# Kernel optimization log

Hardware: AMD Instinct MI355X
Metric: run time of the kernel (lower is better)

## Reference

```python
import jax, jax.numpy as jnp
import numpy as np

B, T, D = 512, 200, 64
VU, VI = 100000, 200000


def _init_params():
    ks = jax.random.split(jax.random.key(1), 12)
    g = lambda k, s, sc=0.05: jax.random.normal(k, s, dtype=jnp.float32) * sc
    return {
        "emb_user": g(ks[0], (VU, D)),
        "emb_item": g(ks[1], (VI, D)),
        "gru_Wx": g(ks[2], (D, 3 * D)),
        "gru_Wh": g(ks[3], (D, 3 * D)),
        "gru_b": jnp.zeros((3 * D,), jnp.float32),
        "aug_Wx": g(ks[4], (D, 3 * D)),
        "aug_Wh": g(ks[5], (D, 3 * D)),
        "aug_b": jnp.zeros((3 * D,), jnp.float32),
        "aux_W1": g(ks[6], (2 * D, 100)),
        "aux_b1": jnp.zeros((100,), jnp.float32),
        "aux_W2": g(ks[7], (100, 50)),
        "aux_b2": jnp.zeros((50,), jnp.float32),
        "aux_W3": g(ks[8], (50, 2)),
        "aux_b3": jnp.zeros((2,), jnp.float32),
        "bn_gamma": jnp.ones((2 * D,), jnp.float32),
        "bn_beta": jnp.zeros((2 * D,), jnp.float32),
        "fc_W1": g(ks[9], (2 * D, 200)),
        "fc_b1": jnp.zeros((200,), jnp.float32),
        "prelu_a1": jnp.zeros((200,), jnp.float32),
        "fc_W2": g(ks[10], (200, 80)),
        "fc_b2": jnp.zeros((80,), jnp.float32),
        "prelu_a2": jnp.zeros((80,), jnp.float32),
        "fc_W3": g(ks[11], (80, 2)),
        "fc_b3": jnp.zeros((2,), jnp.float32),
    }


def setup_inputs():
    key = jax.random.key(0)
    k1, k2, k3 = jax.random.split(key, 3)
    inp = {
        "user_ids": jax.random.randint(k1, (B,), 0, VU),
        "behavior_ids": jax.random.randint(k2, (B, T), 0, VI),
        "target_ids": jax.random.randint(k3, (B,), 0, VI),
    }
    inp.update(_init_params())
    return inp


def _gru(x, Wx, Wh, b):
    # x: [B,T,D]; precompute all input-side gate projections, scan over time
    xg = jnp.einsum("btd,de->bte", x, Wx) + b  # [B,T,3D]

    def step(h, xg_t):
        hg = h @ Wh[:, : 2 * D]
        z = jax.nn.sigmoid(xg_t[:, :D] + hg[:, :D])
        r = jax.nn.sigmoid(xg_t[:, D : 2 * D] + hg[:, D:])
        n = jnp.tanh(xg_t[:, 2 * D :] + (r * h) @ Wh[:, 2 * D :])
        h_new = z * h + (1.0 - z) * n
        return h_new, h_new

    h0 = jnp.zeros((x.shape[0], D), x.dtype)
    _, hs = jax.lax.scan(step, h0, jnp.swapaxes(xg, 0, 1))
    return jnp.swapaxes(hs, 0, 1)  # [B,T,D]


def _augru(x, att, Wx, Wh, b):
    # AUGRU: update gate scaled by attention score; returns final hidden [B,D]
    xg = jnp.einsum("btd,de->bte", x, Wx) + b

    def step(h, inputs):
        xg_t, a_t = inputs
        hg = h @ Wh[:, : 2 * D]
        u = jax.nn.sigmoid(xg_t[:, :D] + hg[:, :D])
        r = jax.nn.sigmoid(xg_t[:, D : 2 * D] + hg[:, D:])
        n = jnp.tanh(xg_t[:, 2 * D :] + (r * h) @ Wh[:, 2 * D :])
        u = a_t[:, None] * u
        h_new = (1.0 - u) * h + u * n
        return h_new, None

    h0 = jnp.zeros((x.shape[0], D), x.dtype)
    h, _ = jax.lax.scan(step, h0, (jnp.swapaxes(xg, 0, 1), att.T))
    return h


def _prelu(x, a):
    return jnp.maximum(x, 0.0) + a * jnp.minimum(x, 0.0)


def _forward(user_ids, behavior_ids, target_ids, p):
    user_emb = p["emb_user"][user_ids]          # [B,D]
    beh_emb = p["emb_item"][behavior_ids]       # [B,T,D]
    tgt_emb = p["emb_item"][target_ids]         # [B,D]

    gru_out = _gru(beh_emb, p["gru_Wx"], p["gru_Wh"], p["gru_b"])  # [B,T,D]

    # auxiliary loss: small MLP on (hidden, behavior emb) pairs, click class prob
    aux_in = jnp.concatenate([gru_out, beh_emb], axis=-1)  # [B,T,2D]
    h1 = jax.nn.relu(aux_in @ p["aux_W1"] + p["aux_b1"])
    h2 = jax.nn.relu(h1 @ p["aux_W2"] + p["aux_b2"])
    aux_logits = h2 @ p["aux_W3"] + p["aux_b3"]  # [B,T,2]
    aux_loss = -jnp.mean(jax.nn.log_softmax(aux_logits, axis=-1)[..., 0])

    # target-item attention over GRU hidden states (softmax over time)
    scores = jnp.einsum("bd,btd->bt", tgt_emb, gru_out)
    att = jax.nn.softmax(scores, axis=-1)  # [B,T]

    h_final = _augru(gru_out, att, p["aug_Wx"], p["aug_Wh"], p["aug_b"])  # [B,D]

    join = jnp.concatenate([h_final, user_emb], axis=-1)  # [B,2D]
    mu = jnp.mean(join, axis=0)
    var = jnp.var(join, axis=0)
    x = (join - mu) * jax.lax.rsqrt(var + 1e-3) * p["bn_gamma"] + p["bn_beta"]
    x = _prelu(jax.nn.relu(x @ p["fc_W1"] + p["fc_b1"]), p["prelu_a1"])
    x = _prelu(jax.nn.relu(x @ p["fc_W2"] + p["fc_b2"]), p["prelu_a2"])
    logit = x @ p["fc_W3"] + p["fc_b3"]  # [B,2]
    output = jax.nn.softmax(logit, axis=-1)
    return output, logit, aux_loss


def reference(user_ids, behavior_ids, target_ids, emb_user, emb_item, gru_Wx, gru_Wh, gru_b, aug_Wx, aug_Wh, aug_b, aux_W1, aux_b1, aux_W2, aux_b2, aux_W3, aux_b3, bn_gamma, bn_beta, fc_W1, fc_b1, prelu_a1, fc_W2, fc_b2, prelu_a2, fc_W3, fc_b3):
    p = dict(emb_user=emb_user, emb_item=emb_item, gru_Wx=gru_Wx, gru_Wh=gru_Wh, gru_b=gru_b,
             aug_Wx=aug_Wx, aug_Wh=aug_Wh, aug_b=aug_b, aux_W1=aux_W1, aux_b1=aux_b1,
             aux_W2=aux_W2, aux_b2=aux_b2, aux_W3=aux_W3, aux_b3=aux_b3,
             bn_gamma=bn_gamma, bn_beta=bn_beta, fc_W1=fc_W1, fc_b1=fc_b1, prelu_a1=prelu_a1,
             fc_W2=fc_W2, fc_b2=fc_b2, prelu_a2=prelu_a2, fc_W3=fc_W3, fc_b3=fc_b3)
    return _forward(user_ids, behavior_ids, target_ids, p)
```

## Files before the change

kernel.cpp:

```cpp
#include <hip/hip_runtime.h>
#include <hip/hip_bf16.h>
#include <math.h>

#define BB 512
#define TT 200
#define DD 64
#define G3 192
#define BT (BB*TT)

typedef __hip_bfloat16 bf16;
typedef short short8 __attribute__((ext_vector_type(8)));
typedef float f32x4 __attribute__((ext_vector_type(4)));

__device__ __forceinline__ float b2f(bf16 v){ return __bfloat162float(v); }
__device__ __forceinline__ float sigm(float x){ x = fminf(fmaxf(x,-30.f),30.f); return 1.f/(1.f+__expf(-x)); }
__device__ __forceinline__ float tanh_(float x){ x = fminf(fmaxf(x,-15.f),15.f); float e=__expf(2.f*x); return (e-1.f)/(e+1.f); }

__device__ __forceinline__ float ldv(const void* p, long i, int isbf){
  if (isbf) return __bfloat162float(((const bf16*)p)[i]);
  return ((const float*)p)[i];
}
__device__ __forceinline__ short f2bs(float f){
  union { bf16 b; short s; } u; u.b = __float2bfloat16(f); return u.s;
}
__device__ __forceinline__ float bs2f(short s){
  union { unsigned u; float f; } x; x.u = ((unsigned)(unsigned short)s) << 16; return x.f;
}
__device__ __forceinline__ float rdlane(float v, int l){
  return __int_as_float(__builtin_amdgcn_readlane(__float_as_int(v), l));
}

__global__ void k_probe(const void* gamma, int* flag){
  if (threadIdx.x==0 && blockIdx.x==0)
    flag[0] = (((const unsigned*)gamma)[0] == 0x3F803F80u) ? 1 : 0;
}

__global__ __launch_bounds__(256) void k_prep(const void* W1, const void* W2, const void* b1,
    const void* b2, const void* W3, const void* b3, const void* gruWx, const void* augWx,
    short* w1t, short* w2t, float* b1f, float* b2f, float* w3f, float* b3f,
    short* wxg, short* wxa, const int* flagp){
  int isbf = *flagp;
  int gid = blockIdx.x*256 + threadIdx.x;
  int gstride = gridDim.x*256;
  for (int i = gid; i < 112*128; i += gstride){
    int n = i >> 7, k = i & 127;
    w1t[i] = f2bs((n < 100) ? ldv(W1, (long)k*100 + n, isbf) : 0.f);
  }
  for (int i = gid; i < 64*128; i += gstride){
    int n = i >> 7, k = i & 127;
    w2t[i] = f2bs((n < 50 && k < 100) ? ldv(W2, (long)k*50 + n, isbf) : 0.f);
  }
  for (int i = gid; i < 12288; i += gstride){
    int j = i & 7, L = (i >> 3) & 63, tk = i >> 9;
    int tile = tk >> 1, kb = tk & 1;
    int k = kb*32 + (L>>4)*8 + j, col = tile*16 + (L & 15);
    wxg[i] = f2bs(ldv(gruWx, (long)k*G3 + col, isbf));
    wxa[i] = f2bs(ldv(augWx, (long)k*G3 + col, isbf));
  }
  if (gid < 112) b1f[gid] = (gid < 100) ? ldv(b1, gid, isbf) : 0.f;
  if (gid < 64)  b2f[gid] = (gid < 50)  ? ldv(b2, gid, isbf) : 0.f;
  if (gid < 100) w3f[gid] = ldv(W3, gid, isbf);
  if (gid < 2)   b3f[gid] = ldv(b3, gid, isbf);
}

__global__ void k_gather(const int* __restrict__ uid, const int* __restrict__ tgt_id,
                         const void* __restrict__ eu, const void* __restrict__ ei,
                         float* __restrict__ tgt, float* __restrict__ usr, const int* flagp){
  int b = blockIdx.x, j = threadIdx.x;
  int isbf = *flagp;
  tgt[b*DD+j] = ldv(ei, (long)tgt_id[b]*DD + j, isbf);
  usr[b*DD+j] = ldv(eu, (long)uid[b]*DD + j, isbf);
}

template<bool GATHER>
__global__ __launch_bounds__(256) void k_xg(const short* __restrict__ wxf, const void* __restrict__ bias,
        const void* __restrict__ emb, const int* __restrict__ ids, const float* __restrict__ Ain,
        float* __restrict__ out, const int* flagp){
  __shared__ __align__(16) char lds[58112];
  int isbf = *flagp;
  int tid = threadIdx.x;
  long rbase = (long)blockIdx.x * 128;
  for (int i = tid; i < 1536; i += 256)
    *(short8*)(lds + i*16) = *(const short8*)(wxf + i*8);
  float* sB = (float*)(lds + 57344);
  if (tid < G3) sB[tid] = ldv(bias, tid, isbf);
  for (int u = tid; u < 1024; u += 256){
    int row = u >> 3, slot = u & 7;
    int off = row*128 + slot*16; off ^= (row&7)<<4;
    if (GATHER){
      long e = (long)ids[rbase+row]*DD + slot*8;
      short8 v;
      if (isbf) v = *(const short8*)((const short*)emb + e);
      else {
        const float* g = (const float*)emb + e;
        f32x4 f0 = *(const f32x4*)g;
        f32x4 f1 = *(const f32x4*)(g+4);
        v[0]=f2bs(f0[0]); v[1]=f2bs(f0[1]); v[2]=f2bs(f0[2]); v[3]=f2bs(f0[3]);
        v[4]=f2bs(f1[0]); v[5]=f2bs(f1[1]); v[6]=f2bs(f1[2]); v[7]=f2bs(f1[3]);
      }
      *(short8*)(lds + 24576 + off) = v;
    } else {
      const float* g = Ain + (rbase+row)*DD + slot*8;
      f32x4 f0 = *(const f32x4*)g;
      f32x4 f1 = *(const f32x4*)(g+4);
      short8 hi, lo;
      #pragma unroll
      for (int q=0;q<4;q++){
        hi[q] = f2bs(f0[q]); lo[q] = f2bs(f0[q] - bs2f(hi[q]));
        hi[4+q] = f2bs(f1[q]); lo[4+q] = f2bs(f1[q] - bs2f(hi[4+q]));
      }
      *(short8*)(lds + 24576 + off) = hi;
      *(short8*)(lds + 40960 + off) = lo;
    }
  }
  __syncthreads();
  int lane = tid & 63, w = tid >> 6;
  int m0 = w*32, lr = lane & 15, lg = lane >> 4;
  f32x4 acc[2][12];
  #pragma unroll
  for (int mi=0;mi<2;mi++){
    #pragma unroll
    for (int nt=0;nt<12;nt++){ acc[mi][nt][0]=0.f; acc[mi][nt][1]=0.f; acc[mi][nt][2]=0.f; acc[mi][nt][3]=0.f; }
  }
  #pragma unroll
  for (int ks=0; ks<2; ks++){
    short8 ah[2], al[2];
    #pragma unroll
    for (int mi=0; mi<2; mi++){
      int row = m0 + mi*16 + lr;
      int off = row*128 + ks*64 + lg*16; off ^= (row&7)<<4;
      ah[mi] = *(const short8*)(lds + 24576 + off);
      if (!GATHER) al[mi] = *(const short8*)(lds + 40960 + off);
    }
    #pragma unroll
    for (int nt=0; nt<12; nt++){
      short8 bf = *(const short8*)(lds + ((nt*2+ks)*64 + lane)*16);
      #pragma unroll
      for (int mi=0; mi<2; mi++){
        if (!GATHER) acc[mi][nt] = __builtin_amdgcn_mfma_f32_16x16x32_bf16(al[mi], bf, acc[mi][nt], 0,0,0);
        acc[mi][nt] = __builtin_amdgcn_mfma_f32_16x16x32_bf16(ah[mi], bf, acc[mi][nt], 0,0,0);
      }
    }
  }
  int r4 = lg*4;
  #pragma unroll
  for (int mi=0;mi<2;mi++){
    #pragma unroll
    for (int nt=0;nt<12;nt++){
      int n = nt*16 + lr;
      float bv = sB[n];
      #pragma unroll
      for (int i=0;i<4;i++){
        long row = rbase + m0 + mi*16 + r4 + i;
        out[row*G3 + n] = acc[mi][nt][i] + bv;
      }
    }
  }
}

template<bool AUG>
__global__ __launch_bounds__(64,1) void k_scan(const float* __restrict__ xg, const void* __restrict__ Whv,
    const float* __restrict__ att, float* __restrict__ hs_out, float* __restrict__ h_final,
    const int* flagp){
  int b = blockIdx.x, j = threadIdx.x;
  int isbf = *flagp;
  float whz[64], whr[64], whn[64];
  if (isbf){
    const bf16* Wh = (const bf16*)Whv;
    #pragma unroll
    for (int d=0; d<64; d++){
      whz[d] = b2f(Wh[d*G3 + j]);
      whr[d] = b2f(Wh[d*G3 + 64 + j]);
      whn[d] = b2f(Wh[d*G3 + 128 + j]);
    }
  } else {
    const float* Wh = (const float*)Whv;
    #pragma unroll
    for (int d=0; d<64; d++){
      whz[d] = Wh[d*G3 + j];
      whr[d] = Wh[d*G3 + 64 + j];
      whn[d] = Wh[d*G3 + 128 + j];
    }
  }
  float hj = 0.f;
  const float* xgb = xg + (size_t)b*TT*G3 + j;
  const float* attb = att + (size_t)b*TT;
  float xz = xgb[0], xr = xgb[64], xn = xgb[128];
  float at = AUG ? attb[0] : 0.f;
  for (int t=0; t<TT; t++){
    int tp = (t+1 < TT) ? t+1 : t;
    const float* q = xgb + (size_t)tp*G3;
    float nxz = q[0], nxr = q[64], nxn = q[128];
    float nat = AUG ? attb[tp] : 0.f;
    float az0=0.f,az1=0.f,az2=0.f,az3=0.f, ar0=0.f,ar1=0.f,ar2=0.f,ar3=0.f;
    #pragma unroll
    for (int d=0; d<64; d+=4){
      float h0=rdlane(hj,d+0), h1=rdlane(hj,d+1), h2=rdlane(hj,d+2), h3=rdlane(hj,d+3);
      az0+=h0*whz[d+0]; az1+=h1*whz[d+1]; az2+=h2*whz[d+2]; az3+=h3*whz[d+3];
      ar0+=h0*whr[d+0]; ar1+=h1*whr[d+1]; ar2+=h2*whr[d+2]; ar3+=h3*whr[d+3];
    }
    float z = sigm(xz + ((az0+az1)+(az2+az3)));
    float r = sigm(xr + ((ar0+ar1)+(ar2+ar3)));
    float u = AUG ? (at*z) : z;
    float rh = r*hj;
    float an0=0.f,an1=0.f,an2=0.f,an3=0.f;
    #pragma unroll
    for (int d=0; d<64; d+=4){
      float r0=rdlane(rh,d+0), r1=rdlane(rh,d+1), r2=rdlane(rh,d+2), r3=rdlane(rh,d+3);
      an0+=r0*whn[d+0]; an1+=r1*whn[d+1]; an2+=r2*whn[d+2]; an3+=r3*whn[d+3];
    }
    float n = tanh_(xn + ((an0+an1)+(an2+an3)));
    float hnew = AUG ? ((1.f-u)*hj + u*n) : (u*hj + (1.f-u)*n);
    hj = hnew;
    if (!AUG) hs_out[((size_t)b*TT + t)*DD + j] = hnew;
    xz=nxz; xr=nxr; xn=nxn; at=nat;
  }
  if (AUG) h_final[b*DD + j] = hj;
}

__global__ __launch_bounds__(256) void k_att(const float* __restrict__ gru, const float* __restrict__ tgt,
                                             float* __restrict__ att){
  int b = blockIdx.x, tid = threadIdx.x;
  __shared__ float st[DD];
  __shared__ float red[256];
  if (tid < DD) st[tid] = tgt[b*DD + tid];
  __syncthreads();
  float s = 0.f;
  if (tid < TT){
    const float* g = gru + ((size_t)b*TT + tid)*DD;
    #pragma unroll
    for (int d=0; d<DD; d++) s += g[d]*st[d];
  }
  red[tid] = (tid<TT) ? s : -1e30f;
  __syncthreads();
  for (int w=128; w>0; w>>=1){ if (tid<w) red[tid] = fmaxf(red[tid], red[tid+w]); __syncthreads(); }
  float m = red[0];
  __syncthreads();
  float e = (tid<TT) ? __expf(s - m) : 0.f;
  red[tid] = e; __syncthreads();
  for (int w=128; w>0; w>>=1){ if (tid<w) red[tid] += red[tid+w]; __syncthreads(); }
  float inv = 1.f/red[0];
  if (tid < TT) att[b*TT + tid] = e*inv;
}

__global__ __launch_bounds__(256) void k_aux(const float* __restrict__ gru, const void* __restrict__ emb,
    const int* __restrict__ ids, const short* __restrict__ w1t, const short* __restrict__ w2t,
    const float* __restrict__ b1f, const float* __restrict__ b2f, const float* __restrict__ w3f,
    const float* __restrict__ b3f, float* __restrict__ part, const int* flagp){
  __shared__ __align__(16) char smem[78976];
  float* sb1 = (float*)(smem + 77824);
  float* sb2 = (float*)(smem + 78272);
  float* sw3 = (float*)(smem + 78528);
  float* sb3 = (float*)(smem + 78928);
  float* wred= (float*)(smem + 78936);
  int tid = threadIdx.x;
  int isbf = *flagp;
  long rbase = (long)blockIdx.x * 128;

  for (int i = tid; i < 1792; i += 256){
    int n = i >> 4, slot = i & 15;
    short8 v = *(const short8*)(w1t + n*128 + slot*8);
    int off = n*256 + slot*16; off ^= (n&7)<<4;
    *(short8*)(smem + 32768 + off) = v;
  }
  for (int i = tid; i < 1024; i += 256){
    int n = i >> 4, slot = i & 15;
    short8 v = *(const short8*)(w2t + n*128 + slot*8);
    int off = n*256 + slot*16; off ^= (n&7)<<4;
    *(short8*)(smem + 61440 + off) = v;
  }
  if (tid < 112) sb1[tid] = b1f[tid];
  if (tid < 100) sw3[tid] = w3f[tid];
  if (tid >= 112 && tid < 176) sb2[tid-112] = b2f[tid-112];
  if (tid >= 176 && tid < 178) sb3[tid-176] = b3f[tid-176];
  for (int i = tid; i < 2048; i += 256){
    int row = i >> 4, slot = i & 15, k0 = slot*8;
    short8 v;
    if (k0 < 64){
      const float* g = gru + (rbase+row)*64 + k0;
      f32x4 f0 = *(const f32x4*)g;
      f32x4 f1 = *(const f32x4*)(g+4);
      v[0]=f2bs(f0[0]); v[1]=f2bs(f0[1]); v[2]=f2bs(f0[2]); v[3]=f2bs(f0[3]);
      v[4]=f2bs(f1[0]); v[5]=f2bs(f1[1]); v[6]=f2bs(f1[2]); v[7]=f2bs(f1[3]);
    } else {
      long e = (long)ids[rbase+row]*64 + (k0-64);
      if (isbf){
        v = *(const short8*)((const short*)emb + e);
      } else {
        const float* g = (const float*)emb + e;
        f32x4 f0 = *(const f32x4*)g;
        f32x4 f1 = *(const f32x4*)(g+4);
        v[0]=f2bs(f0[0]); v[1]=f2bs(f0[1]); v[2]=f2bs(f0[2]); v[3]=f2bs(f0[3]);
        v[4]=f2bs(f1[0]); v[5]=f2bs(f1[1]); v[6]=f2bs(f1[2]); v[7]=f2bs(f1[3]);
      }
    }
    int off = row*256 + slot*16; off ^= (row&7)<<4;
    *(short8*)(smem + off) = v;
  }
  __syncthreads();

  int lane = tid & 63;
  int wv = tid >> 6;
  int m0 = wv * 32;
  int lrow = lane & 15;
  int kbL = ((lane >> 4) * 8) * 2;

  f32x4 acc1[2][7];
  #pragma unroll
  for (int mi=0;mi<2;mi++){
    #pragma unroll
    for (int ni=0;ni<7;ni++){ acc1[mi][ni][0]=0.f; acc1[mi][ni][1]=0.f; acc1[mi][ni][2]=0.f; acc1[mi][ni][3]=0.f; }
  }
  #pragma unroll
  for (int ks=0; ks<4; ks++){
    int kb = ks*64 + kbL;
    short8 af[2], bfv[7];
    #pragma unroll
    for (int mi=0; mi<2; mi++){
      int row = m0 + mi*16 + lrow;
      int off = row*256 + kb; off ^= (row&7)<<4;
      af[mi] = *(const short8*)(smem + off);
    }
    #pragma unroll
    for (int ni=0; ni<7; ni++){
      int n = ni*16 + lrow;
      int off = n*256 + kb; off ^= (n&7)<<4;
      bfv[ni] = *(const short8*)(smem + 32768 + off);
    }
    #pragma unroll
    for (int mi=0; mi<2; mi++){
      #pragma unroll
      for (int ni=0; ni<7; ni++)
        acc1[mi][ni] = __builtin_amdgcn_mfma_f32_16x16x32_bf16(af[mi], bfv[ni], acc1[mi][ni], 0, 0, 0);
    }
  }
  int lr4 = (lane >> 4) * 4;
  #pragma unroll
  for (int mi=0; mi<2; mi++){
    #pragma unroll
    for (int ni=0; ni<7; ni++){
      int col = ni*16 + lrow;
      float bias = sb1[col];
      #pragma unroll
      for (int i=0;i<4;i++){
        int row = m0 + mi*16 + lr4 + i;
        float v = fmaxf(acc1[mi][ni][i] + bias, 0.f);
        int off = row*256 + col*2; off ^= (row&7)<<4;
        *(short*)(smem + off) = f2bs(v);
      }
    }
  }
  {
    int row = m0 + (lane >> 1);
    int off = row*256 + (112 + (lane&1)*8)*2; off ^= (row&7)<<4;
    short8 z = {0,0,0,0,0,0,0,0};
    *(short8*)(smem + off) = z;
  }
  __syncthreads();

  f32x4 acc2[2][4];
  #pragma unroll
  for (int mi=0;mi<2;mi++){
    #pragma unroll
    for (int ni=0;ni<4;ni++){ acc2[mi][ni][0]=0.f; acc2[mi][ni][1]=0.f; acc2[mi][ni][2]=0.f; acc2[mi][ni][3]=0.f; }
  }
  #pragma unroll
  for (int ks=0; ks<4; ks++){
    int kb = ks*64 + kbL;
    short8 af[2], bgv[4];
    #pragma unroll
    for (int mi=0; mi<2; mi++){
      int row = m0 + mi*16 + lrow;
      int off = row*256 + kb; off ^= (row&7)<<4;
      af[mi] = *(const short8*)(smem + off);
    }
    #pragma unroll
    for (int ni=0; ni<4; ni++){
      int n = ni*16 + lrow;
      int off = n*256 + kb; off ^= (n&7)<<4;
      bgv[ni] = *(const short8*)(smem + 61440 + off);
    }
    #pragma unroll
    for (int mi=0; mi<2; mi++){
      #pragma unroll
      for (int ni=0; ni<4; ni++)
        acc2[mi][ni] = __builtin_amdgcn_mfma_f32_16x16x32_bf16(af[mi], bgv[ni], acc2[mi][ni], 0, 0, 0);
    }
  }
  #pragma unroll
  for (int mi=0; mi<2; mi++){
    #pragma unroll
    for (int ni=0; ni<4; ni++){
      int col = ni*16 + lrow;
      float bias = sb2[col];
      #pragma unroll
      for (int i=0;i<4;i++){
        int row = m0 + mi*16 + lr4 + i;
        float v = fmaxf(acc2[mi][ni][i] + bias, 0.f);
        *(short*)(smem + 32768 + row*136 + col*2) = f2bs(v);
      }
    }
  }
  __syncthreads();

  int row = tid >> 1, half = tid & 1;
  const short* h2r = (const short*)(smem + 32768) + row*68;
  float p0 = 0.f, p1 = 0.f;
  int kb0 = half*32, kb1 = half ? 50 : 32;
  for (int k=kb0; k<kb1; k++){
    float h = bs2f(h2r[k]);
    p0 += h*sw3[2*k]; p1 += h*sw3[2*k+1];
  }
  p0 += __shfl_xor(p0, 1, 64);
  p1 += __shfl_xor(p1, 1, 64);
  float l0 = p0 + sb3[0], l1 = p1 + sb3[1];
  float mx = fmaxf(l0, l1);
  float lse = mx + logf(__expf(l0-mx) + __expf(l1-mx));
  float c = (lse - l0) * 0.5f;
  #pragma unroll
  for (int off=32; off; off>>=1) c += __shfl_down(c, off, 64);
  if (lane == 0) wred[wv] = c;
  __syncthreads();
  if (tid == 0) part[blockIdx.x] = wred[0]+wred[1]+wred[2]+wred[3];
}

__global__ void k_auxred(const float* __restrict__ part, float* __restrict__ total){
  __shared__ float red[256];
  int tid = threadIdx.x;
  float s = 0.f;
  for (int i=tid; i<800; i+=256) s += part[i];
  red[tid]=s; __syncthreads();
  for (int w=128;w;w>>=1){ if(tid<w) red[tid]+=red[tid+w]; __syncthreads(); }
  if (tid==0) total[0]=red[0];
}

__global__ __launch_bounds__(64) void k_bn(const float* __restrict__ hf, const float* __restrict__ usr,
                                           float* __restrict__ bn){
  int c = blockIdx.x, l = threadIdx.x;
  const float* src = (c<64) ? (hf + c) : (usr + (c-64));
  float s=0.f, q=0.f;
  for (int r=l; r<BB; r+=64){ float v = src[(size_t)r*DD]; s+=v; q+=v*v; }
  #pragma unroll
  for (int off=32; off; off>>=1){ s += __shfl_down(s,off,64); q += __shfl_down(q,off,64); }
  if (l==0){
    float mean = s*(1.f/BB);
    float var = fmaxf(q*(1.f/BB) - mean*mean, 0.f);
    bn[c] = mean;
    bn[128+c] = rsqrtf(var + 1e-3f);
  }
}

template<typename WT>
__device__ __forceinline__ void fc_body(int b, int tid, const float* hf, const float* usr, const float* bn,
   const WT* gamma, const WT* beta, const WT* W1, const WT* b1, const WT* W2, const WT* b2,
   const WT* W3, const WT* b3, const float* auxsum, void* outv, int obf,
   float* xn, float* y1, float* y2){
  for (int c=tid; c<128; c+=64){
    float v = (c<64) ? hf[b*DD+c] : usr[b*DD + c-64];
    xn[c] = (v - bn[c])*bn[128+c]*b2f(gamma[c]) + b2f(beta[c]);
  }
  __syncthreads();
  #pragma unroll
  for (int i=0;i<4;i++){
    int n = tid + i*64;
    if (n < 200){
      float a = b2f(b1[n]);
      for (int k=0;k<128;k++) a += xn[k]*b2f(W1[k*200+n]);
      y1[n] = fmaxf(a, 0.f);
    }
  }
  __syncthreads();
  #pragma unroll
  for (int i=0;i<2;i++){
    int n = tid + i*64;
    if (n < 80){
      float a = b2f(b2[n]);
      for (int k=0;k<200;k++) a += y1[k]*b2f(W2[k*80+n]);
      y2[n] = fmaxf(a, 0.f);
    }
  }
  __syncthreads();
  float hv = y2[tid];
  float p0 = hv*b2f(W3[tid*2+0]);
  float p1 = hv*b2f(W3[tid*2+1]);
  if (tid < 16){
    float h2 = y2[tid+64];
    p0 += h2*b2f(W3[(tid+64)*2+0]);
    p1 += h2*b2f(W3[(tid+64)*2+1]);
  }
  #pragma unroll
  for (int off=32; off; off>>=1){ p0 += __shfl_down(p0,off,64); p1 += __shfl_down(p1,off,64); }
  if (tid==0){
    float l0 = p0 + b2f(b3[0]), l1 = p1 + b2f(b3[1]);
    float m = fmaxf(l0,l1);
    float e0 = __expf(l0-m), e1 = __expf(l1-m);
    float inv = 1.f/(e0+e1);
    float q0 = e0*inv, q1 = e1*inv;
    float al = auxsum[0] * (1.f/(float)BT);
    if (obf){
      bf16* o = (bf16*)outv;
      o[b*2+0] = __float2bfloat16(q0); o[b*2+1] = __float2bfloat16(q1);
      o[1024 + b*2+0] = __float2bfloat16(l0); o[1024 + b*2+1] = __float2bfloat16(l1);
      if (b==0) o[2048] = __float2bfloat16(al);
    } else {
      float* o = (float*)outv;
      o[b*2+0] = q0; o[b*2+1] = q1;
      o[1024 + b*2+0] = l0; o[1024 + b*2+1] = l1;
      if (b==0) o[2048] = al;
    }
  }
}

__global__ __launch_bounds__(64) void k_fc(const float* __restrict__ hf, const float* __restrict__ usr,
   const float* __restrict__ bn, const void* gamma, const void* beta,
   const void* W1, const void* b1, const void* W2, const void* b2,
   const void* W3, const void* b3, const float* __restrict__ auxsum,
   void* outv, const int* flagp){
  __shared__ float xn[128], y1[200], y2[80];
  int b = blockIdx.x, tid = threadIdx.x;
  int isbf = *flagp;
  if (isbf)
    fc_body<bf16>(b,tid,hf,usr,bn,(const bf16*)gamma,(const bf16*)beta,(const bf16*)W1,(const bf16*)b1,
                  (const bf16*)W2,(const bf16*)b2,(const bf16*)W3,(const bf16*)b3,auxsum,outv,1,xn,y1,y2);
  else
    fc_body<float>(b,tid,hf,usr,bn,(const float*)gamma,(const float*)beta,(const float*)W1,(const float*)b1,
                  (const float*)W2,(const float*)b2,(const float*)W3,(const float*)b3,auxsum,outv,0,xn,y1,y2);
}

extern "C" void kernel_launch(void* const* d_in, const int* in_sizes, int n_in,
                              void* d_out, int out_size, void* d_ws, size_t ws_size,
                              hipStream_t stream) {
  const int*  user_ids     = (const int*) d_in[0];
  const int*  behavior_ids = (const int*) d_in[1];
  const int*  target_ids   = (const int*) d_in[2];
  const void* emb_user = d_in[3];
  const void* emb_item = d_in[4];
  const void* gru_Wx   = d_in[5];
  const void* gru_Wh   = d_in[6];
  const void* gru_b    = d_in[7];
  const void* aug_Wx   = d_in[8];
  const void* aug_Wh   = d_in[9];
  const void* aug_b    = d_in[10];
  const void* aux_W1   = d_in[11];
  const void* aux_b1   = d_in[12];
  const void* aux_W2   = d_in[13];
  const void* aux_b2   = d_in[14];
  const void* aux_W3   = d_in[15];
  const void* aux_b3   = d_in[16];
  const void* bn_gamma = d_in[17];
  const void* bn_beta  = d_in[18];
  const void* fc_W1    = d_in[19];
  const void* fc_b1    = d_in[20];
  const void* fc_W2    = d_in[22];
  const void* fc_b2    = d_in[23];
  const void* fc_W3    = d_in[25];
  const void* fc_b3    = d_in[26];

  float* ws = (float*)d_ws;
  const size_t FLAG_OFF = 0;
  const size_t XG_OFF   = 16;
  const size_t GRU_OFF  = XG_OFF  + (size_t)BT*G3;
  const size_t ATT_OFF  = GRU_OFF + (size_t)BT*DD;
  const size_t TGT_OFF  = ATT_OFF + (size_t)BT;
  const size_t USR_OFF  = TGT_OFF + (size_t)BB*DD;
  const size_t HF_OFF   = USR_OFF + (size_t)BB*DD;
  const size_t BN_OFF   = HF_OFF  + (size_t)BB*DD;
  const size_t AUXP_OFF = BN_OFF  + 256;
  const size_t AUXS_OFF = AUXP_OFF + 800;
  const size_t W1T_OFF  = AUXS_OFF + 16;
  const size_t W2T_OFF  = W1T_OFF + 7168;
  const size_t B1F_OFF  = W2T_OFF + 4096;
  const size_t B2F_OFF  = B1F_OFF + 112;
  const size_t W3F_OFF  = B2F_OFF + 64;
  const size_t B3F_OFF  = W3F_OFF + 100;
  const size_t WXG_OFF  = B3F_OFF + 4;
  const size_t WXA_OFF  = WXG_OFF + 6144;
  const size_t END_OFF  = WXA_OFF + 6144;
  if (ws_size < END_OFF*sizeof(float)) return;

  int*   flag = (int*)(ws + FLAG_OFF);
  float* xg   = ws + XG_OFF;
  float* gruo = ws + GRU_OFF;
  float* att  = ws + ATT_OFF;
  float* tgt  = ws + TGT_OFF;
  float* usr  = ws + USR_OFF;
  float* hf   = ws + HF_OFF;
  float* bnst = ws + BN_OFF;
  float* auxp = ws + AUXP_OFF;
  float* auxs = ws + AUXS_OFF;
  short* w1t  = (short*)(ws + W1T_OFF);
  short* w2t  = (short*)(ws + W2T_OFF);
  float* b1f  = ws + B1F_OFF;
  float* b2f  = ws + B2F_OFF;
  float* w3f  = ws + W3F_OFF;
  float* b3f  = ws + B3F_OFF;
  short* wxg  = (short*)(ws + WXG_OFF);
  short* wxa  = (short*)(ws + WXA_OFF);

  k_probe<<<1, 64, 0, stream>>>(bn_gamma, flag);
  k_prep<<<8, 256, 0, stream>>>(aux_W1, aux_W2, aux_b1, aux_b2, aux_W3, aux_b3, gru_Wx, aug_Wx,
                                w1t, w2t, b1f, b2f, w3f, b3f, wxg, wxa, flag);
  k_gather<<<BB, 64, 0, stream>>>(user_ids, target_ids, emb_user, emb_item, tgt, usr, flag);
  k_xg<true><<<BT/128, 256, 0, stream>>>(wxg, gru_b, emb_item, behavior_ids, nullptr, xg, flag);
  k_scan<false><<<BB, 64, 0, stream>>>(xg, gru_Wh, nullptr, gruo, nullptr, flag);
  k_att<<<BB, 256, 0, stream>>>(gruo, tgt, att);
  k_aux<<<BT/128, 256, 0, stream>>>(gruo, emb_item, behavior_ids, w1t, w2t, b1f, b2f, w3f, b3f, auxp, flag);
  k_auxred<<<1, 256, 0, stream>>>(auxp, auxs);
  k_xg<false><<<BT/128, 256, 0, stream>>>(wxa, aug_b, nullptr, nullptr, gruo, xg, flag);
  k_scan<true><<<BB, 64, 0, stream>>>(xg, aug_Wh, att, nullptr, hf, flag);
  k_bn<<<128, 64, 0, stream>>>(hf, usr, bnst);
  k_fc<<<BB, 64, 0, stream>>>(hf, usr, bnst, bn_gamma, bn_beta, fc_W1, fc_b1, fc_W2, fc_b2, fc_W3, fc_b3, auxs, d_out, flag);
}
```

Before: 451.2 us.

## Compute GRU/AUGRU recurrent matvec with bf16 MFMA instead of readlane FMAs

The per-timestep recurrent h@Wh product in the scan kernel moves from scalar readlane broadcasts plus FMAs to MFMA 16x16x32 bf16 instructions. Wh is held in registers as bf16 fragments, and the hidden state is rearranged into A-fragments with ds_bpermute and rounded to bf16. Only one row of each 16x16 output is used, so most of the MFMA work is wasted. Rounding h and Wh to bf16 inside the recurrence also lowers precision and may let error build up over 200 steps.

```diff
diff --git a/kernel.cpp b/kernel.cpp
--- a/kernel.cpp
+++ b/kernel.cpp
@@ -26,8 +26,26 @@
 __device__ __forceinline__ float bs2f(short s){
   union { unsigned u; float f; } x; x.u = ((unsigned)(unsigned short)s) << 16; return x.f;
 }
-__device__ __forceinline__ float rdlane(float v, int l){
-  return __int_as_float(__builtin_amdgcn_readlane(__float_as_int(v), l));
+__device__ __forceinline__ unsigned pk2(int a, int b){
+  return (((unsigned)a + 0x8000u) >> 16) | (((unsigned)b + 0x8000u) & 0xffff0000u);
+}
+__device__ __forceinline__ short8 gfrag(int bits, int base){
+  int v0 = __builtin_amdgcn_ds_bpermute(base+ 0, bits);
+  int v1 = __builtin_amdgcn_ds_bpermute(base+ 4, bits);
+  int v2 = __builtin_amdgcn_ds_bpermute(base+ 8, bits);
+  int v3 = __builtin_amdgcn_ds_bpermute(base+12, bits);
+  int v4 = __builtin_amdgcn_ds_bpermute(base+16, bits);
+  int v5 = __builtin_amdgcn_ds_bpermute(base+20, bits);
+  int v6 = __builtin_amdgcn_ds_bpermute(base+24, bits);
+  int v7 = __builtin_amdgcn_ds_bpermute(base+28, bits);
+  union { unsigned u[4]; short8 s; } cv;
+  cv.u[0] = pk2(v0,v1); cv.u[1] = pk2(v2,v3); cv.u[2] = pk2(v4,v5); cv.u[3] = pk2(v6,v7);
+  return cv.s;
+}
+__device__ __forceinline__ float sel4(float a0, float a1, float a2, float a3, int lg){
+  float x01 = (lg & 1) ? a1 : a0;
+  float x23 = (lg & 1) ? a3 : a2;
+  return (lg & 2) ? x23 : x01;
 }
 
 __global__ void k_probe(const void* gamma, int* flag){
@@ -162,60 +180,86 @@
 __global__ __launch_bounds__(64,1) void k_scan(const float* __restrict__ xg, const void* __restrict__ Whv,
     const float* __restrict__ att, float* __restrict__ hs_out, float* __restrict__ h_final,
     const int* flagp){
-  int b = blockIdx.x, j = threadIdx.x;
+  int lane = threadIdx.x;
+  int b = blockIdx.x;
   int isbf = *flagp;
-  float whz[64], whr[64], whn[64];
-  if (isbf){
-    const bf16* Wh = (const bf16*)Whv;
-    #pragma unroll
-    for (int d=0; d<64; d++){
-      whz[d] = b2f(Wh[d*G3 + j]);
-      whr[d] = b2f(Wh[d*G3 + 64 + j]);
-      whn[d] = b2f(Wh[d*G3 + 128 + j]);
-    }
-  } else {
-    const float* Wh = (const float*)Whv;
-    #pragma unroll
-    for (int d=0; d<64; d++){
-      whz[d] = Wh[d*G3 + j];
-      whr[d] = Wh[d*G3 + 64 + j];
-      whn[d] = Wh[d*G3 + 128 + j];
+  int lr = lane & 15, lg = lane >> 4;
+  short8 wzf[4][2], wrf[4][2], wnf[4][2];
+  #pragma unroll
+  for (int ti=0; ti<4; ti++){
+    #pragma unroll
+    for (int kb=0; kb<2; kb++){
+      short8 z8, r8, n8;
+      #pragma unroll
+      for (int jj=0; jj<8; jj++){
+        long k = kb*32 + lg*8 + jj;
+        int cz = ti*16 + lr, cr = 64 + ti*16 + lr, cn = 128 + ti*16 + lr;
+        if (isbf){
+          const short* Wh = (const short*)Whv;
+          z8[jj] = Wh[k*G3 + cz]; r8[jj] = Wh[k*G3 + cr]; n8[jj] = Wh[k*G3 + cn];
+        } else {
+          const float* Wh = (const float*)Whv;
+          z8[jj] = f2bs(Wh[k*G3 + cz]); r8[jj] = f2bs(Wh[k*G3 + cr]); n8[jj] = f2bs(Wh[k*G3 + cn]);
+        }
+      }
+      wzf[ti][kb] = z8; wrf[ti][kb] = r8; wnf[ti][kb] = n8;
     }
   }
   float hj = 0.f;
-  const float* xgb = xg + (size_t)b*TT*G3 + j;
+  const float* xgb = xg + (size_t)b*TT*G3;
   const float* attb = att + (size_t)b*TT;
-  float xz = xgb[0], xr = xgb[64], xn = xgb[128];
+  float xz = xgb[lane], xr = xgb[64+lane], xn = xgb[128+lane];
   float at = AUG ? attb[0] : 0.f;
+  int abase = lg*32;
   for (int t=0; t<TT; t++){
     int tp = (t+1 < TT) ? t+1 : t;
-    const float* q = xgb + (size_t)tp*G3;
-    float nxz = q[0], nxr = q[64], nxn = q[128];
+    const float* q_ = xgb + (size_t)tp*G3;
+    float nxz = q_[lane], nxr = q_[64+lane], nxn = q_[128+lane];
     float nat = AUG ? attb[tp] : 0.f;
-    float az0=0.f,az1=0.f,az2=0.f,az3=0.f, ar0=0.f,ar1=0.f,ar2=0.f,ar3=0.f;
-    #pragma unroll
-    for (int d=0; d<64; d+=4){
-      float h0=rdlane(hj,d+0), h1=rdlane(hj,d+1), h2=rdlane(hj,d+2), h3=rdlane(hj,d+3);
-      az0+=h0*whz[d+0]; az1+=h1*whz[d+1]; az2+=h2*whz[d+2]; az3+=h3*whz[d+3];
-      ar0+=h0*whr[d+0]; ar1+=h1*whr[d+1]; ar2+=h2*whr[d+2]; ar3+=h3*whr[d+3];
-    }
-    float z = sigm(xz + ((az0+az1)+(az2+az3)));
-    float r = sigm(xr + ((ar0+ar1)+(ar2+ar3)));
+    int hbits = __float_as_int(hj);
+    short8 ha0 = gfrag(hbits, abase);
+    short8 ha1 = gfrag(hbits, abase + 128);
+    f32x4 az0={0,0,0,0}, az1={0,0,0,0}, az2={0,0,0,0}, az3={0,0,0,0};
+    f32x4 ar0={0,0,0,0}, ar1={0,0,0,0}, ar2={0,0,0,0}, ar3={0,0,0,0};
+    az0 = __builtin_amdgcn_mfma_f32_16x16x32_bf16(ha0, wzf[0][0], az0, 0,0,0);
+    az1 = __builtin_amdgcn_mfma_f32_16x16x32_bf16(ha0, wzf[1][0], az1, 0,0,0);
+    az2 = __builtin_amdgcn_mfma_f32_16x16x32_bf16(ha0, wzf[2][0], az2, 0,0,0);
+    az3 = __builtin_amdgcn_mfma_f32_16x16x32_bf16(ha0, wzf[3][0], az3, 0,0,0);
+    ar0 = __builtin_amdgcn_mfma_f32_16x16x32_bf16(ha0, wrf[0][0], ar0, 0,0,0);
+    ar1 = __builtin_amdgcn_mfma_f32_16x16x32_bf16(ha0, wrf[1][0], ar1, 0,0,0);
+    ar2 = __builtin_amdgcn_mfma_f32_16x16x32_bf16(ha0, wrf[2][0], ar2, 0,0,0);
+    ar3 = __builtin_amdgcn_mfma_f32_16x16x32_bf16(ha0, wrf[3][0], ar3, 0,0,0);
+    az0 = __builtin_amdgcn_mfma_f32_16x16x32_bf16(ha1, wzf[0][1], az0, 0,0,0);
+    az1 = __builtin_amdgcn_mfma_f32_16x16x32_bf16(ha1, wzf[1][1], az1, 0,0,0);
+    az2 = __builtin_amdgcn_mfma_f32_16x16x32_bf16(ha1, wzf[2][1], az2, 0,0,0);
+    az3 = __builtin_amdgcn_mfma_f32_16x16x32_bf16(ha1, wzf[3][1], az3, 0,0,0);
+    ar0 = __builtin_amdgcn_mfma_f32_16x16x32_bf16(ha1, wrf[0][1], ar0, 0,0,0);
+    ar1 = __builtin_amdgcn_mfma_f32_16x16x32_bf16(ha1, wrf[1][1], ar1, 0,0,0);
+    ar2 = __builtin_amdgcn_mfma_f32_16x16x32_bf16(ha1, wrf[2][1], ar2, 0,0,0);
+    ar3 = __builtin_amdgcn_mfma_f32_16x16x32_bf16(ha1, wrf[3][1], ar3, 0,0,0);
+    float z = sigm(xz + sel4(az0[0], az1[0], az2[0], az3[0], lg));
+    float r = sigm(xr + sel4(ar0[0], ar1[0], ar2[0], ar3[0], lg));
     float u = AUG ? (at*z) : z;
     float rh = r*hj;
-    float an0=0.f,an1=0.f,an2=0.f,an3=0.f;
-    #pragma unroll
-    for (int d=0; d<64; d+=4){
-      float r0=rdlane(rh,d+0), r1=rdlane(rh,d+1), r2=rdlane(rh,d+2), r3=rdlane(rh,d+3);
-      an0+=r0*whn[d+0]; an1+=r1*whn[d+1]; an2+=r2*whn[d+2]; an3+=r3*whn[d+3];
-    }
-    float n = tanh_(xn + ((an0+an1)+(an2+an3)));
+    int rbits = __float_as_int(rh);
+    short8 ra0 = gfrag(rbits, abase);
+    short8 ra1 = gfrag(rbits, abase + 128);
+    f32x4 an0={0,0,0,0}, an1={0,0,0,0}, an2={0,0,0,0}, an3={0,0,0,0};
+    an0 = __builtin_amdgcn_mfma_f32_16x16x32_bf16(ra0, wnf[0][0], an0, 0,0,0);
+    an1 = __builtin_amdgcn_mfma_f32_16x16x32_bf16(ra0, wnf[1][0], an1, 0,0,0);
+    an2 = __builtin_amdgcn_mfma_f32_16x16x32_bf16(ra0, wnf[2][0], an2, 0,0,0);
+    an3 = __builtin_amdgcn_mfma_f32_16x16x32_bf16(ra0, wnf[3][0], an3, 0,0,0);
+    an0 = __builtin_amdgcn_mfma_f32_16x16x32_bf16(ra1, wnf[0][1], an0, 0,0,0);
+    an1 = __builtin_amdgcn_mfma_f32_16x16x32_bf16(ra1, wnf[1][1], an1, 0,0,0);
+    an2 = __builtin_amdgcn_mfma_f32_16x16x32_bf16(ra1, wnf[2][1], an2, 0,0,0);
+    an3 = __builtin_amdgcn_mfma_f32_16x16x32_bf16(ra1, wnf[3][1], an3, 0,0,0);
+    float n = tanh_(xn + sel4(an0[0], an1[0], an2[0], an3[0], lg));
     float hnew = AUG ? ((1.f-u)*hj + u*n) : (u*hj + (1.f-u)*n);
     hj = hnew;
-    if (!AUG) hs_out[((size_t)b*TT + t)*DD + j] = hnew;
+    if (!AUG) hs_out[((size_t)b*TT + t)*DD + lane] = hnew;
     xz=nxz; xr=nxr; xn=nxn; at=nat;
   }
-  if (AUG) h_final[b*DD + j] = hj;
+  if (AUG) h_final[b*DD + lane] = hj;
 }
 
 __global__ __launch_bounds__(256) void k_att(const float* __restrict__ gru, const float* __restrict__ tgt,
```

New measurement: 476.9 us. 1.06x slower.
